# Kernel tuning notes

Hardware: AMD Instinct MI355X
Metric: run time of the kernel (lower is better)

The kernel has to match this reference:

```python
import jax, jax.numpy as jnp
import numpy as np

T, B, E, H = 2048, 2, 1024, 16
HD = E // H  # 64


def _apply_rope(x, sin_pos, cos_pos):
    # x: [B*H, T, HD]; rotate-half interleaved variant
    rot = jnp.stack([-x[..., 1::2], x[..., ::2]], axis=-1).reshape(x.shape)
    return x * cos_pos + rot * sin_pos


def setup_inputs() -> dict:
    key = jax.random.key(0)
    ks = jax.random.split(key, 6)
    scale_in = (6.0 / (3 * E + E)) ** 0.5  # xavier_uniform bound
    scale_out = (6.0 / (E + E)) ** 0.5
    return {
        "query": jax.random.normal(ks[0], (T, B, E), dtype=jnp.float32),
        "rel_pos": jax.random.normal(ks[1], (1, T, HD), dtype=jnp.float32),
        "in_proj_weight": jax.random.uniform(ks[2], (3 * E, E), jnp.float32, -scale_in, scale_in),
        "in_proj_bias": jnp.zeros((3 * E,), jnp.float32),
        "out_proj_weight": jax.random.uniform(ks[3], (E, E), jnp.float32, -scale_out, scale_out),
        "out_proj_bias": jnp.zeros((E,), jnp.float32),
    }


def reference(query, rel_pos, in_proj_weight, in_proj_bias, out_proj_weight, out_proj_bias):
    tgt_len, bsz, embed_dim = query.shape
    scaling = HD ** -0.5
    # fused QKV projection: F.linear(query, W, b) with W [3E, E]
    qkv = jnp.einsum("tbe,fe->tbf", query, in_proj_weight) + in_proj_bias
    q, k, v = jnp.split(qkv, 3, axis=-1)
    q = q * scaling
    # [T, B, E] -> [B*H, T, HD]
    def split_heads(x):
        return jnp.transpose(x.reshape(tgt_len, bsz * H, HD), (1, 0, 2))
    q, k, v = split_heads(q), split_heads(k), split_heads(v)
    # rotary embedding: sin, cos = rel_pos.chunk(2, -1), duplicated interleaved
    sin, cos = rel_pos[..., : HD // 2], rel_pos[..., HD // 2 :]
    sin_pos = jnp.stack([sin, sin], axis=-1).reshape(rel_pos.shape)
    cos_pos = jnp.stack([cos, cos], axis=-1).reshape(rel_pos.shape)
    q = _apply_rope(q, sin_pos, cos_pos)
    k = _apply_rope(k, sin_pos, cos_pos)
    # attention
    attn_weights = jnp.einsum("bqd,bkd->bqk", q, k)  # [B*H, T, T]
    attn_weights = jax.nn.softmax(attn_weights, axis=-1)
    attn = jnp.einsum("bqk,bkd->bqd", attn_weights, v)
    # [B*H, T, HD] -> [T, B, E]
    attn = jnp.transpose(attn, (1, 0, 2)).reshape(tgt_len, bsz, embed_dim)
    out = jnp.einsum("tbe,fe->tbf", attn, out_proj_weight) + out_proj_bias
    return out
```

## Files before the change

kernel.cpp:

```cpp
#include <hip/hip_runtime.h>

#define T_  2048
#define B_  2
#define E_  1024
#define H_  16
#define HD_ 64
#define M_  4096
#define N_QKV 3072

typedef unsigned short u16;
typedef unsigned int   u32;
typedef __attribute__((ext_vector_type(8))) __bf16 bf16x8;
typedef __attribute__((ext_vector_type(4))) float  f32x4;

__device__ inline u16 f2bf(float f) {
  u32 u = __float_as_uint(f);
  u += 0x7fffu + ((u >> 16) & 1u);
  return (u16)(u >> 16);
}

__device__ inline u32 cvtpk(float lo, float hi) {
  u32 r;
  asm("v_cvt_pk_bf16_f32 %0, %1, %2" : "=v"(r) : "v"(lo), "v"(hi));
  return r;
}

__device__ inline float ex2(float x) {
#if __has_builtin(__builtin_amdgcn_exp2f)
  return __builtin_amdgcn_exp2f(x);
#else
  return __expf(x * 0.69314718f);
#endif
}

__device__ inline void gl_lds16(const u16* g, u16* l) {
  __builtin_amdgcn_global_load_lds(
      (const __attribute__((address_space(1))) u32*)g,
      (__attribute__((address_space(3))) u32*)l, 16, 0, 0);
}

__device__ inline int xcd_swz(int orig, int nwg) {
  return (orig & 7) * (nwg >> 3) + (orig >> 3);
}

__global__ __launch_bounds__(256) void cvt_kernel(
    const float* __restrict__ q, const float* __restrict__ wi,
    const float* __restrict__ wo, u16* __restrict__ X,
    u16* __restrict__ Wi, u16* __restrict__ Wo) {
  int idx = blockIdx.x * 256 + threadIdx.x;
  const int n1 = (M_ * E_) / 4, n2 = (3 * E_ * E_) / 4;
  const float4* src; u16* dst; int i;
  if (idx < n1)            { src = (const float4*)q;  dst = X;  i = idx; }
  else if (idx < n1 + n2)  { src = (const float4*)wi; dst = Wi; i = idx - n1; }
  else                     { src = (const float4*)wo; dst = Wo; i = idx - n1 - n2; }
  float4 v = src[i];
  uint2 o;
  o.x = (u32)f2bf(v.x) | ((u32)f2bf(v.y) << 16);
  o.y = (u32)f2bf(v.z) | ((u32)f2bf(v.w) << 16);
  *(uint2*)&dst[(size_t)i * 4] = o;
}

__global__ __launch_bounds__(512) void gemm_qkv(
    const u16* __restrict__ X, const u16* __restrict__ W,
    const float* __restrict__ bias, const float* __restrict__ rel,
    u16* __restrict__ qb, u16* __restrict__ kp, u16* __restrict__ vp) {
  const int K = E_;
  __shared__ u16 SH[16384];
  u16 (*As)[4096] = (u16(*)[4096])SH;
  u16 (*Bs)[4096] = (u16(*)[4096])(SH + 8192);
  int orig = blockIdx.y * gridDim.x + blockIdx.x;
  int wgid = xcd_swz(orig, 32 * 24);
  const int tm = (wgid & 31) * 128, tn = (wgid >> 5) * 128;
  const int tid = threadIdx.x;
  const int w = tid >> 6, lane = tid & 63, lr = lane & 15, lg = lane >> 4;
  const int wm = (w >> 2) * 64, wn = (w & 3) * 32;
  auto stage = [&](int buf, int k0) {
    int ca = tid;
    int ga = ca ^ ((ca >> 3) & 3);
    gl_lds16(X + (size_t)(tm + (ga >> 2)) * K + k0 + (ga & 3) * 8,
             &As[buf][ca * 8]);
    gl_lds16(W + (size_t)(tn + (ga >> 2)) * K + k0 + (ga & 3) * 8,
             &Bs[buf][ca * 8]);
  };
  f32x4 acc[4][2] = {};
  stage(0, 0);
  __syncthreads();
  for (int it = 0; it < 32; ++it) {
    int cur = it & 1;
    if (it < 31) stage(cur ^ 1, (it + 1) * 32);
    bf16x8 af[4], bq[2];
    #pragma unroll
    for (int mi = 0; mi < 4; ++mi) {
      int ga = (wm + mi * 16 + lr) * 4 + lg; ga ^= (ga >> 3) & 3;
      af[mi] = *(const bf16x8*)&As[cur][ga * 8];
    }
    #pragma unroll
    for (int ni = 0; ni < 2; ++ni) {
      int ga = (wn + ni * 16 + lr) * 4 + lg; ga ^= (ga >> 3) & 3;
      bq[ni] = *(const bf16x8*)&Bs[cur][ga * 8];
    }
    #pragma unroll
    for (int mi = 0; mi < 4; ++mi)
      #pragma unroll
      for (int ni = 0; ni < 2; ++ni)
        acc[mi][ni] = __builtin_amdgcn_mfma_f32_16x16x32_bf16(
            af[mi], bq[ni], acc[mi][ni], 0, 0, 0);
    __syncthreads();
  }
  const int sect = tn >> 10;
  #pragma unroll
  for (int ni = 0; ni < 2; ++ni) {
    int n = tn + wn + ni * 16 + lr;
    float bv = bias[n];
    int nn = n & 1023;
    int d = nn & 63, i2 = d >> 1;
    int hsub = (nn >> 6) & 1;
    #pragma unroll
    for (int mi = 0; mi < 4; ++mi) {
      #pragma unroll
      for (int r = 0; r < 4; ++r) {
        int m = tm + wm + mi * 16 + lg * 4 + r;
        int t = m >> 1, bb = m & 1, tl = t & 63;
        float v = acc[mi][ni][r] + bv;
        if (sect == 0) v *= 0.18033688f;
        if (sect < 2) {
          float partner = __shfl_xor(v, 1);
          float sp = rel[t * HD_ + i2];
          float cp = rel[t * HD_ + 32 + i2];
          float rot = (d & 1) ? partner : -partner;
          v = v * cp + rot * sp;
        }
        int off;
        if (sect == 0)
          off = tl * 64 + d;
        else if (sect == 1)
          off = (((tl >> 4) * 2 + (d >> 5)) << 9)
              + (((d >> 3) & 3) << 7) + ((tl & 15) << 3) + (d & 7);
        else
          off = (((tl >> 5) * 4 + (d >> 4)) << 9)
              + (((tl >> 3) & 3) << 7) + ((d & 15) << 3) + (tl & 7);
        SH[((bb << 1) | hsub) * 4096 + off] = f2bf(v);
      }
    }
  }
  __syncthreads();
  {
    int h0 = (tn & 1023) >> 6;
    int c = w >> 1, half = w & 1;
    int bb = c >> 1, hs = c & 1;
    int bh = bb * H_ + h0 + hs;
    int t0 = tm >> 1;
    u16* dst;
    if (sect == 0)      dst = qb + ((size_t)bh * T_ + t0) * HD_;
    else if (sect == 1) dst = kp + (((size_t)bh * 32 + (t0 >> 6)) << 12);
    else                dst = vp + (((size_t)bh * 32 + (t0 >> 6)) << 12);
    const u16* srcp = SH + c * 4096;
    #pragma unroll
    for (int i = 0; i < 4; ++i) {
      int g = half * 256 + i * 64 + lane;
      *(uint4*)&dst[(size_t)g * 8] = *(const uint4*)&srcp[g * 8];
    }
  }
}

__global__ __launch_bounds__(512) void attn_kernel(
    const u16* __restrict__ qbm, const u16* __restrict__ kp,
    const u16* __restrict__ vp, u16* __restrict__ attnb) {
  __shared__ u16 Kl[2][8192];
  __shared__ u16 Vl[2][8192];
  int orig = blockIdx.y * gridDim.x + blockIdx.x;
  int wgid = xcd_swz(orig, 16 * 32);
  int bh = wgid >> 4;
  int tid = threadIdx.x;
  int w = tid >> 6, lane = tid & 63, lr = lane & 15, lg = lane >> 4;
  int qbase = (wgid & 15) * 128 + w * 16;
  const u16* qrow  = qbm + (size_t)bh * T_ * HD_;
  const u16* ktile = kp + ((size_t)bh * 32) * 4096;
  const u16* vtile = vp + ((size_t)bh * 32) * 4096;
  bf16x8 qf[2];
  #pragma unroll
  for (int ks = 0; ks < 2; ++ks)
    qf[ks] = *(const bf16x8*)&qrow[(size_t)(qbase + lr) * HD_ + ks * 32 + lg * 8];
  auto stage = [&](int buf, int kt) {
    const u16* kn = ktile + ((size_t)kt) * 8192;
    const u16* vn = vtile + ((size_t)kt) * 8192;
    gl_lds16(kn + (size_t)tid * 8,         &Kl[buf][(w * 64) * 8]);
    gl_lds16(kn + (size_t)(tid + 512) * 8, &Kl[buf][(w * 64 + 512) * 8]);
    gl_lds16(vn + (size_t)tid * 8,         &Vl[buf][(w * 64) * 8]);
    gl_lds16(vn + (size_t)(tid + 512) * 8, &Vl[buf][(w * 64 + 512) * 8]);
  };
  f32x4 o[4] = {};
  float mrun = -INFINITY, lrun = 0.f;
  stage(0, 0);
  __syncthreads();
  for (int kt = 0; kt < 16; ++kt) {
    int cur = kt & 1;
    if (kt < 15) stage(cur ^ 1, kt + 1);
    f32x4 st[8];
    __builtin_amdgcn_s_setprio(1);
    #pragma unroll
    for (int kb4 = 0; kb4 < 8; ++kb4) {
      st[kb4] = (f32x4){0.f, 0.f, 0.f, 0.f};
      #pragma unroll
      for (int ks = 0; ks < 2; ++ks) {
        bf16x8 a = *(const bf16x8*)&Kl[cur][(kb4 * 2 + ks) * 512 + lane * 8];
        st[kb4] = __builtin_amdgcn_mfma_f32_16x16x32_bf16(a, qf[ks], st[kb4], 0, 0, 0);
      }
    }
    __builtin_amdgcn_s_setprio(0);
    float mm[8];
    #pragma unroll
    for (int kb4 = 0; kb4 < 8; ++kb4)
      mm[kb4] = fmaxf(fmaxf(st[kb4][0], st[kb4][1]),
                      fmaxf(st[kb4][2], st[kb4][3]));
    float mxl = fmaxf(fmaxf(fmaxf(mm[0], mm[1]), fmaxf(mm[2], mm[3])),
                      fmaxf(fmaxf(mm[4], mm[5]), fmaxf(mm[6], mm[7])));
    if (!__all(mxl <= mrun + 11.5f)) {
      float mx = fmaxf(mxl, __shfl_xor(mxl, 16));
      mx = fmaxf(mx, __shfl_xor(mx, 32));
      float mnew = fmaxf(mrun, mx);
      float sc = ex2(mrun - mnew);
      lrun *= sc;
      #pragma unroll
      for (int db = 0; db < 4; ++db) o[db] *= sc;
      mrun = mnew;
    }
    u32 cv[8][2];
    float s01 = 0.f, s23 = 0.f;
    #pragma unroll
    for (int kb4 = 0; kb4 < 8; ++kb4) {
      float p0 = ex2(st[kb4][0] - mrun);
      float p1 = ex2(st[kb4][1] - mrun);
      float p2 = ex2(st[kb4][2] - mrun);
      float p3 = ex2(st[kb4][3] - mrun);
      if (kb4 & 2) s23 += (p0 + p1) + (p2 + p3);
      else         s01 += (p0 + p1) + (p2 + p3);
      cv[kb4][0] = cvtpk(p0, p1);
      cv[kb4][1] = cvtpk(p2, p3);
    }
    lrun += s01 + s23;
    #pragma unroll
    for (int ks = 0; ks < 4; ++ks) {
      u32 a = cv[ks * 2][0], b = cv[ks * 2][1];
      u32 c = cv[ks * 2 + 1][0], d = cv[ks * 2 + 1][1];
      asm("v_permlane32_swap_b32 %0, %1" : "+v"(a), "+v"(c));
      asm("v_permlane32_swap_b32 %0, %1" : "+v"(b), "+v"(d));
      asm("v_permlane16_swap_b32 %0, %1" : "+v"(a), "+v"(c));
      asm("v_permlane16_swap_b32 %0, %1" : "+v"(b), "+v"(d));
      u32 pf32[4] = {a, b, c, d};
      bf16x8 pf = *(const bf16x8*)pf32;
      __builtin_amdgcn_s_setprio(1);
      #pragma unroll
      for (int db = 0; db < 4; ++db) {
        bf16x8 vf = *(const bf16x8*)&Vl[cur][(ks * 4 + db) * 512 + lane * 8];
        o[db] = __builtin_amdgcn_mfma_f32_16x16x32_bf16(vf, pf, o[db], 0, 0, 0);
      }
      __builtin_amdgcn_s_setprio(0);
    }
    __syncthreads();
  }
  lrun += __shfl_xor(lrun, 16);
  lrun += __shfl_xor(lrun, 32);
  float inv = 1.f / lrun;
  int bb = bh >> 4, h = bh & 15;
  int m = (qbase + lr) * 2 + bb;
  #pragma unroll
  for (int db = 0; db < 4; ++db) {
    uint2 u;
    u.x = cvtpk(o[db][0] * inv, o[db][1] * inv);
    u.y = cvtpk(o[db][2] * inv, o[db][3] * inv);
    *(uint2*)&attnb[(size_t)m * E_ + h * 64 + db * 16 + lg * 4] = u;
  }
}

__global__ __launch_bounds__(256) void gemm_out(
    const u16* __restrict__ A, const u16* __restrict__ W,
    const float* __restrict__ bias, float* __restrict__ out) {
  const int K = E_;
  __shared__ u16 As[2][2048];
  __shared__ u16 Bs[2][2048];
  int orig = blockIdx.y * gridDim.x + blockIdx.x;
  int wgid = xcd_swz(orig, 64 * 16);
  const int tm = (wgid & 63) * 64, tn = (wgid >> 6) * 64;
  const int tid = threadIdx.x;
  const int w = tid >> 6, lane = tid & 63, lr = lane & 15, lg = lane >> 4;
  const int wm = (w >> 1) * 32, wn = (w & 1) * 32;
  auto stage = [&](int buf, int k0) {
    int ca = w * 64 + lane;
    int ga = ca ^ ((ca >> 3) & 3);
    gl_lds16(A + (size_t)(tm + (ga >> 2)) * K + k0 + (ga & 3) * 8,
             &As[buf][ca * 8]);
    gl_lds16(W + (size_t)(tn + (ga >> 2)) * K + k0 + (ga & 3) * 8,
             &Bs[buf][ca * 8]);
  };
  f32x4 acc[2][2] = {};
  stage(0, 0);
  __syncthreads();
  for (int it = 0; it < 32; ++it) {
    int cur = it & 1;
    if (it < 31) stage(cur ^ 1, (it + 1) * 32);
    bf16x8 af[2], bq[2];
    #pragma unroll
    for (int mi = 0; mi < 2; ++mi) {
      int ga = (wm + mi * 16 + lr) * 4 + lg; ga ^= (ga >> 3) & 3;
      af[mi] = *(const bf16x8*)&As[cur][ga * 8];
    }
    #pragma unroll
    for (int ni = 0; ni < 2; ++ni) {
      int gb = (wn + ni * 16 + lr) * 4 + lg; gb ^= (gb >> 3) & 3;
      bq[ni] = *(const bf16x8*)&Bs[cur][gb * 8];
    }
    #pragma unroll
    for (int mi = 0; mi < 2; ++mi)
      #pragma unroll
      for (int ni = 0; ni < 2; ++ni)
        acc[mi][ni] = __builtin_amdgcn_mfma_f32_16x16x32_bf16(
            af[mi], bq[ni], acc[mi][ni], 0, 0, 0);
    __syncthreads();
  }
  #pragma unroll
  for (int ni = 0; ni < 2; ++ni) {
    int n = tn + wn + ni * 16 + lr;
    float bv = bias[n];
    #pragma unroll
    for (int mi = 0; mi < 2; ++mi) {
      #pragma unroll
      for (int r = 0; r < 4; ++r) {
        int m = tm + wm + mi * 16 + lg * 4 + r;
        out[(size_t)m * E_ + n] = acc[mi][ni][r] + bv;
      }
    }
  }
}

extern "C" void kernel_launch(void* const* d_in, const int* in_sizes, int n_in,
                              void* d_out, int out_size, void* d_ws, size_t ws_size,
                              hipStream_t stream) {
  const float* q   = (const float*)d_in[0];
  const float* rel = (const float*)d_in[1];
  const float* wi  = (const float*)d_in[2];
  const float* bi  = (const float*)d_in[3];
  const float* wo  = (const float*)d_in[4];
  const float* bo  = (const float*)d_in[5];
  float* out = (float*)d_out;
  char* ws = (char*)d_ws;
  u16* Xb  = (u16*)(ws);
  u16* Wib = (u16*)(ws + 8388608);
  u16* Wob = (u16*)(ws + 14680064);
  u16* qb  = (u16*)(ws + 16777216);
  u16* kpb = (u16*)(ws + 25165824);
  u16* vpb = (u16*)(ws + 33554432);
  u16* attnb = Xb;

  cvt_kernel<<<dim3(8192), dim3(256), 0, stream>>>(q, wi, wo, Xb, Wib, Wob);
  gemm_qkv<<<dim3(32, 24), dim3(512), 0, stream>>>(Xb, Wib, bi, rel, qb, kpb, vpb);
  attn_kernel<<<dim3(16, 32), dim3(512), 0, stream>>>(qb, kpb, vpb, attnb);
  gemm_out<<<dim3(64, 16), dim3(256), 0, stream>>>(attnb, Wob, bo, out);
}
```

Measured before the change: 122.1 us.

## Fuse fp32-to-bf16 conversion of query into QKV GEMM A-tile loads

The query activation is no longer converted to bf16 by a separate pass. The QKV GEMM now streams fp32 query tiles straight into LDS with a new XOR swizzle and converts them to bf16 with v_cvt_pk_bf16_f32 when building MFMA fragments. This removes a full read and write of the 16MB activation and shrinks the conversion kernel. In exchange the GEMM reads twice the A bytes per K-step, uses more LDS (48KB), and does conversion work repeated across the 24 N-tiles.

```diff
diff --git a/kernel.cpp b/kernel.cpp
--- a/kernel.cpp
+++ b/kernel.cpp
@@ -44,15 +44,13 @@
 }
 
 __global__ __launch_bounds__(256) void cvt_kernel(
-    const float* __restrict__ q, const float* __restrict__ wi,
-    const float* __restrict__ wo, u16* __restrict__ X,
+    const float* __restrict__ wi, const float* __restrict__ wo,
     u16* __restrict__ Wi, u16* __restrict__ Wo) {
   int idx = blockIdx.x * 256 + threadIdx.x;
-  const int n1 = (M_ * E_) / 4, n2 = (3 * E_ * E_) / 4;
+  const int n1 = (3 * E_ * E_) / 4;
   const float4* src; u16* dst; int i;
-  if (idx < n1)            { src = (const float4*)q;  dst = X;  i = idx; }
-  else if (idx < n1 + n2)  { src = (const float4*)wi; dst = Wi; i = idx - n1; }
-  else                     { src = (const float4*)wo; dst = Wo; i = idx - n1 - n2; }
+  if (idx < n1) { src = (const float4*)wi; dst = Wi; i = idx; }
+  else          { src = (const float4*)wo; dst = Wo; i = idx - n1; }
   float4 v = src[i];
   uint2 o;
   o.x = (u32)f2bf(v.x) | ((u32)f2bf(v.y) << 16);
@@ -61,13 +59,13 @@
 }
 
 __global__ __launch_bounds__(512) void gemm_qkv(
-    const u16* __restrict__ X, const u16* __restrict__ W,
+    const float* __restrict__ X, const u16* __restrict__ W,
     const float* __restrict__ bias, const float* __restrict__ rel,
     u16* __restrict__ qb, u16* __restrict__ kp, u16* __restrict__ vp) {
   const int K = E_;
-  __shared__ u16 SH[16384];
-  u16 (*As)[4096] = (u16(*)[4096])SH;
-  u16 (*Bs)[4096] = (u16(*)[4096])(SH + 8192);
+  __shared__ u16 SH[24576];
+  float* Afp = (float*)SH;
+  u16 (*Bs)[4096] = (u16(*)[4096])(SH + 16384);
   int orig = blockIdx.y * gridDim.x + blockIdx.x;
   int wgid = xcd_swz(orig, 32 * 24);
   const int tm = (wgid & 31) * 128, tn = (wgid >> 5) * 128;
@@ -75,12 +73,18 @@
   const int w = tid >> 6, lane = tid & 63, lr = lane & 15, lg = lane >> 4;
   const int wm = (w >> 2) * 64, wn = (w & 3) * 32;
   auto stage = [&](int buf, int k0) {
-    int ca = tid;
-    int ga = ca ^ ((ca >> 3) & 3);
-    gl_lds16(X + (size_t)(tm + (ga >> 2)) * K + k0 + (ga & 3) * 8,
-             &As[buf][ca * 8]);
-    gl_lds16(W + (size_t)(tn + (ga >> 2)) * K + k0 + (ga & 3) * 8,
-             &Bs[buf][ca * 8]);
+    #pragma unroll
+    for (int h = 0; h < 2; ++h) {
+      int ca = tid + h * 512;
+      int row = ca >> 3;
+      int lc = (ca & 7) ^ (row & 7);
+      gl_lds16((const u16*)(X + (size_t)(tm + row) * K + k0 + lc * 4),
+               (u16*)(Afp + buf * 4096 + ca * 4));
+    }
+    int cb = tid;
+    int gb = cb ^ ((cb >> 3) & 3);
+    gl_lds16(W + (size_t)(tn + (gb >> 2)) * K + k0 + (gb & 3) * 8,
+             &Bs[buf][cb * 8]);
   };
   f32x4 acc[4][2] = {};
   stage(0, 0);
@@ -91,8 +95,14 @@
     bf16x8 af[4], bq[2];
     #pragma unroll
     for (int mi = 0; mi < 4; ++mi) {
-      int ga = (wm + mi * 16 + lr) * 4 + lg; ga ^= (ga >> 3) & 3;
-      af[mi] = *(const bf16x8*)&As[cur][ga * 8];
+      int row = wm + mi * 16 + lr;
+      int s = row & 7;
+      const float* rp = Afp + cur * 4096 + row * 32;
+      f32x4 lo = *(const f32x4*)(rp + ((lg * 2) ^ s) * 4);
+      f32x4 hi = *(const f32x4*)(rp + ((lg * 2 + 1) ^ s) * 4);
+      u32 fr[4] = {cvtpk(lo[0], lo[1]), cvtpk(lo[2], lo[3]),
+                   cvtpk(hi[0], hi[1]), cvtpk(hi[2], hi[3])};
+      af[mi] = *(const bf16x8*)fr;
     }
     #pragma unroll
     for (int ni = 0; ni < 2; ++ni) {
@@ -344,16 +354,15 @@
   const float* bo  = (const float*)d_in[5];
   float* out = (float*)d_out;
   char* ws = (char*)d_ws;
-  u16* Xb  = (u16*)(ws);
   u16* Wib = (u16*)(ws + 8388608);
   u16* Wob = (u16*)(ws + 14680064);
   u16* qb  = (u16*)(ws + 16777216);
   u16* kpb = (u16*)(ws + 25165824);
   u16* vpb = (u16*)(ws + 33554432);
-  u16* attnb = Xb;
-
-  cvt_kernel<<<dim3(8192), dim3(256), 0, stream>>>(q, wi, wo, Xb, Wib, Wob);
-  gemm_qkv<<<dim3(32, 24), dim3(512), 0, stream>>>(Xb, Wib, bi, rel, qb, kpb, vpb);
+  u16* attnb = (u16*)ws;
+
+  cvt_kernel<<<dim3(4096), dim3(256), 0, stream>>>(wi, wo, Wib, Wob);
+  gemm_qkv<<<dim3(32, 24), dim3(512), 0, stream>>>(q, Wib, bi, rel, qb, kpb, vpb);
   attn_kernel<<<dim3(16, 32), dim3(512), 0, stream>>>(qb, kpb, vpb, attnb);
   gemm_out<<<dim3(64, 16), dim3(256), 0, stream>>>(attnb, Wob, bo, out);
 }
```

Result: slower. 141.9 us (+16.2%).
